# Kernel tuning notes

Measured on AMD Instinct MI355X. Metric: run time of the kernel, lower is better.

The kernel has to match this reference:

```python
import jax, jax.numpy as jnp
import numpy as np

N_NODES = 50000


def _gcn_norm(edge_index, n_nodes):
    # Add self-loops, then symmetric normalization D^-1/2 (A+I) D^-1/2 (GCNConv default).
    src = jnp.concatenate([edge_index[0], jnp.arange(n_nodes)])
    dst = jnp.concatenate([edge_index[1], jnp.arange(n_nodes)])
    deg = jax.ops.segment_sum(jnp.ones_like(src, dtype=jnp.float32), dst, num_segments=n_nodes)
    dinv = jnp.where(deg > 0, jax.lax.rsqrt(jnp.maximum(deg, 1.0)), 0.0)
    norm = dinv[src] * dinv[dst]  # [E + N]
    return src, dst, norm


def _gcn_conv(x, W, b, src, dst, norm, n_nodes):
    h = x @ W                      # [N, F_out] transform first (fewer bytes moved)
    msg = h[src] * norm[:, None]   # gather per-edge
    out = jax.ops.segment_sum(msg, dst, num_segments=n_nodes)  # scatter-add
    return out + b


def setup_inputs() -> dict:
    key = jax.random.key(0)
    k_x, k_e, k1, k2, k3, k4, k5, k6 = jax.random.split(key, 8)
    in_dim, hid, out_dim, n_edges = 128, 128, 64, 800000
    s = lambda fan_in: 1.0 / np.sqrt(fan_in)
    return {
        "x": jax.random.normal(k_x, (N_NODES, in_dim), dtype=jnp.float32),
        "edge_index": jax.random.randint(k_e, (2, n_edges), 0, N_NODES),
        "W1": jax.random.uniform(k1, (in_dim, hid), jnp.float32, -s(in_dim), s(in_dim)),
        "b1": jnp.zeros((hid,), jnp.float32),
        "W_mu": jax.random.uniform(k2, (hid, out_dim), jnp.float32, -s(hid), s(hid)),
        "b_mu": jnp.zeros((out_dim,), jnp.float32),
        "W_logstd": jax.random.uniform(k3, (hid, out_dim), jnp.float32, -s(hid), s(hid)),
        "b_logstd": jnp.zeros((out_dim,), jnp.float32),
    }


def reference(x, edge_index, W1, b1, W_mu, b_mu, W_logstd, b_logstd):
    src, dst, norm = _gcn_norm(edge_index, N_NODES)
    h = jax.nn.relu(_gcn_conv(x, W1, b1, src, dst, norm, N_NODES))
    mu = _gcn_conv(h, W_mu, b_mu, src, dst, norm, N_NODES)
    logstd = _gcn_conv(h, W_logstd, b_logstd, src, dst, norm, N_NODES)
    return mu, logstd
```

## Files before the change

kernel.cpp:

```cpp
#include <hip/hip_runtime.h>
#include <hip/hip_bf16.h>

#define N_NODES 50000
#define FDIM 128
#define NPAD 50176
#define SCAN_NB 49

typedef short bf16x8 __attribute__((ext_vector_type(8)));
typedef float f32x4  __attribute__((ext_vector_type(4)));

__device__ __forceinline__ unsigned short rne_bf16(float f) {
    unsigned int u = __float_as_uint(f);
    unsigned int r = (u + 0x7FFFu + ((u >> 16) & 1u)) >> 16;
    return (unsigned short)r;
}
__device__ __forceinline__ float bf16_to_f32(unsigned short s) {
    return __uint_as_float(((unsigned int)s) << 16);
}
__device__ __forceinline__ void split_bf16(float f, unsigned short& h, unsigned short& l) {
    h = rne_bf16(f);
    l = rne_bf16(f - bf16_to_f32(h));
}
__device__ __forceinline__ void unpack2(unsigned int d, float& f0, float& f1) {
    f0 = __uint_as_float(d << 16);
    f1 = __uint_as_float(d & 0xFFFF0000u);
}
__device__ __forceinline__ void add_row(const uint4& m, float* a) {
    float f0, f1;
    unpack2(m.x, f0, f1); a[0] += f0; a[1] += f1;
    unpack2(m.y, f0, f1); a[2] += f0; a[3] += f1;
    unpack2(m.z, f0, f1); a[4] += f0; a[5] += f1;
    unpack2(m.w, f0, f1); a[6] += f0; a[7] += f1;
}

__global__ __launch_bounds__(256) void zero_cvtw_kernel(int4* __restrict__ counts4,
                                                        const float* __restrict__ W1,
                                                        const float* __restrict__ Wmu,
                                                        const float* __restrict__ Wlog,
                                                        unsigned short* __restrict__ W1thi,
                                                        unsigned short* __restrict__ W1tlo,
                                                        unsigned short* __restrict__ Wcthi,
                                                        unsigned short* __restrict__ Wctlo) {
    int b = blockIdx.x;
    if (b < SCAN_NB) {
        int i = b * 256 + threadIdx.x;
        if (i < NPAD / 4) counts4[i] = make_int4(0, 0, 0, 0);
        return;
    }
    int tid = (b - SCAN_NB) * 256 + threadIdx.x;
    int n = tid & 127, k = tid >> 7;
    int swzidx = (n * 128 + k) ^ ((n & 7) << 3);
    unsigned short h, l;
    float v1 = W1[k * 128 + n];
    split_bf16(v1, h, l);
    W1thi[swzidx] = h;
    W1tlo[swzidx] = l;
    float v2 = (n < 64) ? Wmu[k * 64 + n] : Wlog[k * 64 + (n - 64)];
    split_bf16(v2, h, l);
    Wcthi[swzidx] = h;
    Wctlo[swzidx] = l;
}

__global__ __launch_bounds__(256) void count_kernel(const int* __restrict__ dst,
                                                    int* __restrict__ counts,
                                                    int* __restrict__ rank, int E) {
    int e = blockIdx.x * blockDim.x + threadIdx.x;
    if (e < E) rank[e] = atomicAdd(&counts[dst[e]], 1);
}

__global__ __launch_bounds__(256) void scan_local_kernel(const int* __restrict__ counts,
                                                         int* __restrict__ local,
                                                         int* __restrict__ bsums,
                                                         float* __restrict__ dinv) {
    int t    = threadIdx.x;
    int lane = t & 63;
    int wid  = t >> 6;
    int base = blockIdx.x * 1024 + t * 4;
    int4 c = *(const int4*)(counts + base);
    float4 dv;
    dv.x = (base + 0 < N_NODES) ? rsqrtf((float)c.x + 1.0f) : 0.f;
    dv.y = (base + 1 < N_NODES) ? rsqrtf((float)c.y + 1.0f) : 0.f;
    dv.z = (base + 2 < N_NODES) ? rsqrtf((float)c.z + 1.0f) : 0.f;
    dv.w = (base + 3 < N_NODES) ? rsqrtf((float)c.w + 1.0f) : 0.f;
    *(float4*)(dinv + base) = dv;
    int4 v;
    v.x = (c.x + 3) & ~3;
    v.y = (c.y + 3) & ~3;
    v.z = (c.z + 3) & ~3;
    v.w = (c.w + 3) & ~3;
    int s = v.x + v.y + v.z + v.w;
    int incl = s;
#pragma unroll
    for (int off = 1; off < 64; off <<= 1) {
        int u = __shfl_up(incl, off, 64);
        if (lane >= off) incl += u;
    }
    __shared__ int wtot[4];
    if (lane == 63) wtot[wid] = incl;
    __syncthreads();
    int wbase = 0;
#pragma unroll
    for (int w = 0; w < 3; w++) wbase += (w < wid) ? wtot[w] : 0;
    int excl = wbase + incl - s;
    int4 o;
    o.x = excl;
    o.y = excl + v.x;
    o.z = o.y + v.y;
    o.w = o.z + v.z;
    *(int4*)(local + base) = o;
    if (t == 255) bsums[blockIdx.x] = wbase + incl;
}

__global__ __launch_bounds__(256) void scan_add_kernel(const int* __restrict__ local,
                                                       const int* __restrict__ bsums,
                                                       const int* __restrict__ counts,
                                                       int* __restrict__ offsets,
                                                       int* __restrict__ csr_src,
                                                       unsigned short* __restrict__ xb,
                                                       unsigned short* __restrict__ Hb) {
    int t = threadIdx.x;
    __shared__ int s_bo;
    if (t < 64) {
        int v = (t < blockIdx.x) ? bsums[t] : 0;
#pragma unroll
        for (int off = 32; off; off >>= 1) v += __shfl_down(v, off, 64);
        if (t == 0) s_bo = v;
    }
    if (blockIdx.x == 0 && t >= 64 && t < 128) {
        int k = t - 64;
        ((unsigned int*)(xb + (size_t)N_NODES * 128))[k] = 0u;
        ((unsigned int*)(Hb + (size_t)N_NODES * 128))[k] = 0u;
    }
    __syncthreads();
    int bo = s_bo;
    int base = blockIdx.x * 1024 + t * 4;
    int4 v = *(const int4*)(local + base);
    int4 c = *(const int4*)(counts + base);
    v.x += bo; v.y += bo; v.z += bo; v.w += bo;
    *(int4*)(offsets + base) = v;
    int off0[4] = {v.x, v.y, v.z, v.w};
    int cr[4]   = {c.x, c.y, c.z, c.w};
#pragma unroll
    for (int k = 0; k < 4; k++) {
        int b = off0[k] + cr[k];
        int e = off0[k] + ((cr[k] + 3) & ~3);
        for (int j = b; j < e; j++) csr_src[j] = N_NODES;
    }
}

__global__ __launch_bounds__(256) void scatter_cvtx_kernel(const int* __restrict__ src,
                                                           const int* __restrict__ dst,
                                                           const int* __restrict__ rank,
                                                           const int* __restrict__ offsets,
                                                           int* __restrict__ csr_src, int E,
                                                           int scb,
                                                           const float* __restrict__ x,
                                                           const float* __restrict__ dinv,
                                                           unsigned short* __restrict__ xb,
                                                           int n4) {
    int b = blockIdx.x;
    if (b < scb) {
        int e = b * 256 + threadIdx.x;
        if (e < E) {
            int d = dst[e];
            int pos = offsets[d] + rank[e];
            csr_src[pos] = src[e];
        }
        return;
    }
    int i = (b - scb) * 256 + threadIdx.x;
    if (i >= n4) return;
    float dv = dinv[i >> 5];
    float4 v = ((const float4*)x)[i];
    v.x *= dv; v.y *= dv; v.z *= dv; v.w *= dv;
    unsigned int d0 = (unsigned int)rne_bf16(v.x) | ((unsigned int)rne_bf16(v.y) << 16);
    unsigned int d1 = (unsigned int)rne_bf16(v.z) | ((unsigned int)rne_bf16(v.w) << 16);
    ((uint2*)xb)[i] = make_uint2(d0, d1);
}

__global__ __launch_bounds__(256) void agg_bf16_kernel(const unsigned short* __restrict__ X,
                                                       const int* __restrict__ offsets,
                                                       const int* __restrict__ csr_src,
                                                       const float* __restrict__ dinv,
                                                       unsigned short* __restrict__ Y,
                                                       int n) {
    int node = (blockIdx.x << 4) + (threadIdx.x >> 4);
    int l16  = threadIdx.x & 15;
    if (node >= n) return;
    const uint4* X16 = (const uint4*)X;

    float a[8];
    {
        uint4 xv = X16[(size_t)node * 16 + l16];
        float f0, f1;
        unpack2(xv.x, f0, f1); a[0] = f0; a[1] = f1;
        unpack2(xv.y, f0, f1); a[2] = f0; a[3] = f1;
        unpack2(xv.z, f0, f1); a[4] = f0; a[5] = f1;
        unpack2(xv.w, f0, f1); a[6] = f0; a[7] = f1;
    }

    int beg = offsets[node], end = offsets[node + 1];
    int i = beg;
    for (; i + 8 <= end; i += 8) {
        int4 q0 = *(const int4*)(csr_src + i);
        int4 q1 = *(const int4*)(csr_src + i + 4);
        uint4 m0 = X16[(size_t)q0.x * 16 + l16];
        uint4 m1 = X16[(size_t)q0.y * 16 + l16];
        uint4 m2 = X16[(size_t)q0.z * 16 + l16];
        uint4 m3 = X16[(size_t)q0.w * 16 + l16];
        uint4 m4 = X16[(size_t)q1.x * 16 + l16];
        uint4 m5 = X16[(size_t)q1.y * 16 + l16];
        uint4 m6 = X16[(size_t)q1.z * 16 + l16];
        uint4 m7 = X16[(size_t)q1.w * 16 + l16];
        add_row(m0, a); add_row(m1, a); add_row(m2, a); add_row(m3, a);
        add_row(m4, a); add_row(m5, a); add_row(m6, a); add_row(m7, a);
    }
    if (i < end) {
        int4 q0 = *(const int4*)(csr_src + i);
        uint4 m0 = X16[(size_t)q0.x * 16 + l16];
        uint4 m1 = X16[(size_t)q0.y * 16 + l16];
        uint4 m2 = X16[(size_t)q0.z * 16 + l16];
        uint4 m3 = X16[(size_t)q0.w * 16 + l16];
        add_row(m0, a); add_row(m1, a); add_row(m2, a); add_row(m3, a);
    }

    float dv = dinv[node];
    unsigned short h[8];
#pragma unroll
    for (int j = 0; j < 8; j++) h[j] = rne_bf16(a[j] * dv);
    uint4 ph;
    ph.x = (unsigned int)h[0] | ((unsigned int)h[1] << 16);
    ph.y = (unsigned int)h[2] | ((unsigned int)h[3] << 16);
    ph.z = (unsigned int)h[4] | ((unsigned int)h[5] << 16);
    ph.w = (unsigned int)h[6] | ((unsigned int)h[7] << 16);
    ((uint4*)Y)[(size_t)node * 16 + l16] = ph;
}

template <int EPI>
__global__ __launch_bounds__(512) void mfma_gemm_kernel(const unsigned short* __restrict__ A,
                                                        const unsigned short* __restrict__ Wthi,
                                                        const unsigned short* __restrict__ Wtlo,
                                                        const float* __restrict__ ba,
                                                        const float* __restrict__ bb,
                                                        const float* __restrict__ dinv,
                                                        unsigned short* __restrict__ H,
                                                        float* __restrict__ out, int M) {
    __shared__ unsigned short Wlds[32768];

    int t    = threadIdx.x;
    int wave = t >> 6;
    int lane = t & 63;
    int m16  = lane & 15;
    int kg   = lane >> 4;

    {
        const uint4* gh = (const uint4*)Wthi;
        const uint4* gl = (const uint4*)Wtlo;
        uint4* lds4 = (uint4*)Wlds;
#pragma unroll
        for (int i = 0; i < 4; i++) lds4[i * 512 + t] = gh[i * 512 + t];
#pragma unroll
        for (int i = 0; i < 4; i++) lds4[2048 + i * 512 + t] = gl[i * 512 + t];
    }

    int rbase = blockIdx.x * 128 + wave * 16;
    int arow  = rbase + m16;
    bool rok  = arow < M;
    const unsigned short* ar = A + (size_t)(rok ? arow : 0) * 128;
    bf16x8 af[4];
#pragma unroll
    for (int kt = 0; kt < 4; kt++) {
        bf16x8 v = *(const bf16x8*)(const void*)(ar + kt * 32 + kg * 8);
        af[kt] = rok ? v : (bf16x8)(short)0;
    }
    float4 dv4 = {1.f, 1.f, 1.f, 1.f};
    if (EPI == 0) dv4 = *(const float4*)(dinv + rbase + kg * 4);
    __syncthreads();

    int swz = (m16 & 7) << 3;
#pragma unroll
    for (int np = 0; np < 4; np++) {
        int nt0 = np * 2, nt1 = np * 2 + 1;
        f32x4 acc0 = {0.f, 0.f, 0.f, 0.f};
        f32x4 acc1 = {0.f, 0.f, 0.f, 0.f};
#pragma unroll
        for (int kt = 0; kt < 4; kt++) {
            int i0 = (((nt0 * 16 + m16) * 128) + kt * 32 + kg * 8) ^ swz;
            int i1 = (((nt1 * 16 + m16) * 128) + kt * 32 + kg * 8) ^ swz;
            bf16x8 bh0 = *(const bf16x8*)(const void*)&Wlds[i0];
            bf16x8 bl0 = *(const bf16x8*)(const void*)&Wlds[16384 + i0];
            bf16x8 bh1 = *(const bf16x8*)(const void*)&Wlds[i1];
            bf16x8 bl1 = *(const bf16x8*)(const void*)&Wlds[16384 + i1];
            acc0 = __builtin_amdgcn_mfma_f32_16x16x32_bf16(af[kt], bh0, acc0, 0, 0, 0);
            acc1 = __builtin_amdgcn_mfma_f32_16x16x32_bf16(af[kt], bh1, acc1, 0, 0, 0);
            acc0 = __builtin_amdgcn_mfma_f32_16x16x32_bf16(af[kt], bl0, acc0, 0, 0, 0);
            acc1 = __builtin_amdgcn_mfma_f32_16x16x32_bf16(af[kt], bl1, acc1, 0, 0, 0);
        }
#pragma unroll
        for (int half = 0; half < 2; half++) {
            int nt = half ? nt1 : nt0;
            const f32x4& acc = half ? acc1 : acc0;
            int n0 = nt * 16 + m16;
            if (EPI == 0) {
                float b = ba[n0];
#pragma unroll
                for (int j = 0; j < 4; j++) {
                    int r = rbase + kg * 4 + j;
                    if (r < M) {
                        float v = fmaxf(acc[j] + b, 0.f) * dv4[j];
                        H[(size_t)r * 128 + n0] = rne_bf16(v);
                    }
                }
            } else {
                bool is_mu = (n0 < 64);
                int c = is_mu ? n0 : (n0 - 64);
                float b = is_mu ? ba[c] : bb[c];
                size_t obase = is_mu ? 0 : (size_t)N_NODES * 64;
#pragma unroll
                for (int j = 0; j < 4; j++) {
                    int r = rbase + kg * 4 + j;
                    if (r < M) out[obase + (size_t)r * 64 + c] = acc[j] + b;
                }
            }
        }
    }
}

extern "C" void kernel_launch(void* const* d_in, const int* in_sizes, int n_in,
                              void* d_out, int out_size, void* d_ws, size_t ws_size,
                              hipStream_t stream) {
    const float* x    = (const float*)d_in[0];
    const int*   ei   = (const int*)d_in[1];
    const float* W1   = (const float*)d_in[2];
    const float* b1   = (const float*)d_in[3];
    const float* Wmu  = (const float*)d_in[4];
    const float* bmu  = (const float*)d_in[5];
    const float* Wlog = (const float*)d_in[6];
    const float* blog = (const float*)d_in[7];
    float* out = (float*)d_out;

    const int N = N_NODES;
    const int E = in_sizes[1] / 2;
    const int Emax = E + 3 * N;
    const int* src = ei;
    const int* dst = ei + E;

    auto align256 = [](size_t v) { return (v + 255) & ~(size_t)255; };
    char* ws = (char*)d_ws;
    size_t off = 0;
    int*   counts  = (int*)(ws + off);  off += align256((size_t)NPAD * 4);
    int*   offsets = (int*)(ws + off);  off += align256((size_t)NPAD * 4);
    int*   local   = (int*)(ws + off);  off += align256((size_t)NPAD * 4);
    int*   bsums   = (int*)(ws + off);  off += align256(256 * 4);
    float* dinv    = (float*)(ws + off); off += align256((size_t)NPAD * 4);
    int*   rank    = (int*)(ws + off);  off += align256((size_t)E * 4);
    int*   csr_src = (int*)(ws + off);  off += align256((size_t)Emax * 4);
    unsigned short* xb    = (unsigned short*)(ws + off); off += align256((size_t)(N + 1) * FDIM * 2);
    unsigned short* Hb    = (unsigned short*)(ws + off); off += align256((size_t)(N + 1) * FDIM * 2);
    unsigned short* Ag    = (unsigned short*)(ws + off); off += align256((size_t)N * FDIM * 2);
    unsigned short* W1thi = (unsigned short*)(ws + off); off += align256(128 * 128 * 2);
    unsigned short* W1tlo = (unsigned short*)(ws + off); off += align256(128 * 128 * 2);
    unsigned short* Wcthi = (unsigned short*)(ws + off); off += align256(128 * 128 * 2);
    unsigned short* Wctlo = (unsigned short*)(ws + off); off += align256(128 * 128 * 2);

    zero_cvtw_kernel<<<SCAN_NB + 64, 256, 0, stream>>>((int4*)counts, W1, Wmu, Wlog,
                                                       W1thi, W1tlo, Wcthi, Wctlo);
    count_kernel<<<(E + 255) / 256, 256, 0, stream>>>(dst, counts, rank, E);
    scan_local_kernel<<<SCAN_NB, 256, 0, stream>>>(counts, local, bsums, dinv);
    scan_add_kernel<<<SCAN_NB, 256, 0, stream>>>(local, bsums, counts, offsets,
                                                 csr_src, xb, Hb);
    {
        int scb = (E + 255) / 256;
        int cvb = (N * FDIM / 4 + 255) / 256;
        scatter_cvtx_kernel<<<scb + cvb, 256, 0, stream>>>(src, dst, rank, offsets,
                                                           csr_src, E, scb,
                                                           x, dinv, xb, N * FDIM / 4);
    }
    agg_bf16_kernel<<<(N + 15) / 16, 256, 0, stream>>>(xb, offsets, csr_src, dinv, Ag, N);
    mfma_gemm_kernel<0><<<(N + 127) / 128, 512, 0, stream>>>(Ag, W1thi, W1tlo,
                                                             b1, nullptr, dinv, Hb, nullptr, N);
    agg_bf16_kernel<<<(N + 15) / 16, 256, 0, stream>>>(Hb, offsets, csr_src, dinv, Ag, N);
    mfma_gemm_kernel<1><<<(N + 127) / 128, 512, 0, stream>>>(Ag, Wcthi, Wctlo,
                                                             bmu, blog, nullptr, nullptr, out, N);
}
```

Measured before the change: 150.7 us.

## Fuse neighbor aggregation into MFMA GEMM kernel, eliminating intermediate buffer

Replaces the separate aggregation and GEMM kernels with one kernel. Each lane gathers and sums the neighbor rows for its own node straight into registers laid out as MFMA A-fragments, then runs the bf16 hi/lo MFMA GEMM. This removes the global write and read of the aggregated matrix and two kernel launches per layer. In exchange each lane now processes a whole 32-float row slice over all edges, which raises register pressure (launch_bounds 512,4). Load balance across nodes of different degree is also coarser than in the 16-lane-per-node aggregation kernel.

New measurement: 286.2 us. 1.9x slower.

```diff
diff --git a/kernel.cpp b/kernel.cpp
--- a/kernel.cpp
+++ b/kernel.cpp
@@ -178,73 +178,18 @@
     ((uint2*)xb)[i] = make_uint2(d0, d1);
 }
 
-__global__ __launch_bounds__(256) void agg_bf16_kernel(const unsigned short* __restrict__ X,
-                                                       const int* __restrict__ offsets,
-                                                       const int* __restrict__ csr_src,
-                                                       const float* __restrict__ dinv,
-                                                       unsigned short* __restrict__ Y,
-                                                       int n) {
-    int node = (blockIdx.x << 4) + (threadIdx.x >> 4);
-    int l16  = threadIdx.x & 15;
-    if (node >= n) return;
-    const uint4* X16 = (const uint4*)X;
-
-    float a[8];
-    {
-        uint4 xv = X16[(size_t)node * 16 + l16];
-        float f0, f1;
-        unpack2(xv.x, f0, f1); a[0] = f0; a[1] = f1;
-        unpack2(xv.y, f0, f1); a[2] = f0; a[3] = f1;
-        unpack2(xv.z, f0, f1); a[4] = f0; a[5] = f1;
-        unpack2(xv.w, f0, f1); a[6] = f0; a[7] = f1;
-    }
-
-    int beg = offsets[node], end = offsets[node + 1];
-    int i = beg;
-    for (; i + 8 <= end; i += 8) {
-        int4 q0 = *(const int4*)(csr_src + i);
-        int4 q1 = *(const int4*)(csr_src + i + 4);
-        uint4 m0 = X16[(size_t)q0.x * 16 + l16];
-        uint4 m1 = X16[(size_t)q0.y * 16 + l16];
-        uint4 m2 = X16[(size_t)q0.z * 16 + l16];
-        uint4 m3 = X16[(size_t)q0.w * 16 + l16];
-        uint4 m4 = X16[(size_t)q1.x * 16 + l16];
-        uint4 m5 = X16[(size_t)q1.y * 16 + l16];
-        uint4 m6 = X16[(size_t)q1.z * 16 + l16];
-        uint4 m7 = X16[(size_t)q1.w * 16 + l16];
-        add_row(m0, a); add_row(m1, a); add_row(m2, a); add_row(m3, a);
-        add_row(m4, a); add_row(m5, a); add_row(m6, a); add_row(m7, a);
-    }
-    if (i < end) {
-        int4 q0 = *(const int4*)(csr_src + i);
-        uint4 m0 = X16[(size_t)q0.x * 16 + l16];
-        uint4 m1 = X16[(size_t)q0.y * 16 + l16];
-        uint4 m2 = X16[(size_t)q0.z * 16 + l16];
-        uint4 m3 = X16[(size_t)q0.w * 16 + l16];
-        add_row(m0, a); add_row(m1, a); add_row(m2, a); add_row(m3, a);
-    }
-
-    float dv = dinv[node];
-    unsigned short h[8];
-#pragma unroll
-    for (int j = 0; j < 8; j++) h[j] = rne_bf16(a[j] * dv);
-    uint4 ph;
-    ph.x = (unsigned int)h[0] | ((unsigned int)h[1] << 16);
-    ph.y = (unsigned int)h[2] | ((unsigned int)h[3] << 16);
-    ph.z = (unsigned int)h[4] | ((unsigned int)h[5] << 16);
-    ph.w = (unsigned int)h[6] | ((unsigned int)h[7] << 16);
-    ((uint4*)Y)[(size_t)node * 16 + l16] = ph;
-}
-
 template <int EPI>
-__global__ __launch_bounds__(512) void mfma_gemm_kernel(const unsigned short* __restrict__ A,
-                                                        const unsigned short* __restrict__ Wthi,
-                                                        const unsigned short* __restrict__ Wtlo,
-                                                        const float* __restrict__ ba,
-                                                        const float* __restrict__ bb,
-                                                        const float* __restrict__ dinv,
-                                                        unsigned short* __restrict__ H,
-                                                        float* __restrict__ out, int M) {
+__global__ __launch_bounds__(512, 4) void fused_agg_gemm_kernel(
+        const unsigned short* __restrict__ X,
+        const int* __restrict__ offsets,
+        const int* __restrict__ csr_src,
+        const float* __restrict__ dinv,
+        const unsigned short* __restrict__ Wthi,
+        const unsigned short* __restrict__ Wtlo,
+        const float* __restrict__ ba,
+        const float* __restrict__ bb,
+        unsigned short* __restrict__ H,
+        float* __restrict__ out, int M) {
     __shared__ unsigned short Wlds[32768];
 
     int t    = threadIdx.x;
@@ -256,25 +201,70 @@
     {
         const uint4* gh = (const uint4*)Wthi;
         const uint4* gl = (const uint4*)Wtlo;
+        uint4 wr[8];
+#pragma unroll
+        for (int i = 0; i < 4; i++) wr[i] = gh[i * 512 + t];
+#pragma unroll
+        for (int i = 0; i < 4; i++) wr[4 + i] = gl[i * 512 + t];
         uint4* lds4 = (uint4*)Wlds;
 #pragma unroll
-        for (int i = 0; i < 4; i++) lds4[i * 512 + t] = gh[i * 512 + t];
-#pragma unroll
-        for (int i = 0; i < 4; i++) lds4[2048 + i * 512 + t] = gl[i * 512 + t];
-    }
-
-    int rbase = blockIdx.x * 128 + wave * 16;
-    int arow  = rbase + m16;
-    bool rok  = arow < M;
-    const unsigned short* ar = A + (size_t)(rok ? arow : 0) * 128;
+        for (int i = 0; i < 4; i++) lds4[i * 512 + t] = wr[i];
+#pragma unroll
+        for (int i = 0; i < 4; i++) lds4[2048 + i * 512 + t] = wr[4 + i];
+    }
+
+    int wrbase = blockIdx.x * 128 + wave * 16;
+    int node   = wrbase + m16;
+    bool rok   = node < M;
+    int snode  = rok ? node : N_NODES;
+    const uint4* X16 = (const uint4*)X;
+
+    float acc[32];
+#pragma unroll
+    for (int kt = 0; kt < 4; kt++) {
+        uint4 s = X16[(size_t)snode * 16 + kt * 4 + kg];
+        float f0, f1;
+        unpack2(s.x, f0, f1); acc[kt * 8 + 0] = f0; acc[kt * 8 + 1] = f1;
+        unpack2(s.y, f0, f1); acc[kt * 8 + 2] = f0; acc[kt * 8 + 3] = f1;
+        unpack2(s.z, f0, f1); acc[kt * 8 + 4] = f0; acc[kt * 8 + 5] = f1;
+        unpack2(s.w, f0, f1); acc[kt * 8 + 6] = f0; acc[kt * 8 + 7] = f1;
+    }
+
+    int beg = offsets[node], end = offsets[node + 1];
+    for (int i = beg; i < end; i += 4) {
+        int4 q = *(const int4*)(csr_src + i);
+        uint4 r0[4], r1[4];
+#pragma unroll
+        for (int kt = 0; kt < 4; kt++) r0[kt] = X16[(size_t)q.x * 16 + kt * 4 + kg];
+#pragma unroll
+        for (int kt = 0; kt < 4; kt++) r1[kt] = X16[(size_t)q.y * 16 + kt * 4 + kg];
+#pragma unroll
+        for (int kt = 0; kt < 4; kt++) add_row(r0[kt], acc + kt * 8);
+#pragma unroll
+        for (int kt = 0; kt < 4; kt++) add_row(r1[kt], acc + kt * 8);
+#pragma unroll
+        for (int kt = 0; kt < 4; kt++) r0[kt] = X16[(size_t)q.z * 16 + kt * 4 + kg];
+#pragma unroll
+        for (int kt = 0; kt < 4; kt++) r1[kt] = X16[(size_t)q.w * 16 + kt * 4 + kg];
+#pragma unroll
+        for (int kt = 0; kt < 4; kt++) add_row(r0[kt], acc + kt * 8);
+#pragma unroll
+        for (int kt = 0; kt < 4; kt++) add_row(r1[kt], acc + kt * 8);
+    }
+
+    float dvn = dinv[node];
     bf16x8 af[4];
 #pragma unroll
     for (int kt = 0; kt < 4; kt++) {
-        bf16x8 v = *(const bf16x8*)(const void*)(ar + kt * 32 + kg * 8);
-        af[kt] = rok ? v : (bf16x8)(short)0;
-    }
+        bf16x8 v;
+#pragma unroll
+        for (int j = 0; j < 8; j++) v[j] = (short)rne_bf16(acc[kt * 8 + j] * dvn);
+        af[kt] = v;
+    }
+
     float4 dv4 = {1.f, 1.f, 1.f, 1.f};
-    if (EPI == 0) dv4 = *(const float4*)(dinv + rbase + kg * 4);
+    if (EPI == 0) dv4 = *(const float4*)(dinv + wrbase + kg * 4);
+
     __syncthreads();
 
     int swz = (m16 & 7) << 3;
@@ -299,15 +289,15 @@
 #pragma unroll
         for (int half = 0; half < 2; half++) {
             int nt = half ? nt1 : nt0;
-            const f32x4& acc = half ? acc1 : acc0;
+            const f32x4& a = half ? acc1 : acc0;
             int n0 = nt * 16 + m16;
             if (EPI == 0) {
                 float b = ba[n0];
 #pragma unroll
                 for (int j = 0; j < 4; j++) {
-                    int r = rbase + kg * 4 + j;
+                    int r = wrbase + kg * 4 + j;
                     if (r < M) {
-                        float v = fmaxf(acc[j] + b, 0.f) * dv4[j];
+                        float v = fmaxf(a[j] + b, 0.f) * dv4[j];
                         H[(size_t)r * 128 + n0] = rne_bf16(v);
                     }
                 }
@@ -318,8 +308,8 @@
                 size_t obase = is_mu ? 0 : (size_t)N_NODES * 64;
 #pragma unroll
                 for (int j = 0; j < 4; j++) {
-                    int r = rbase + kg * 4 + j;
-                    if (r < M) out[obase + (size_t)r * 64 + c] = acc[j] + b;
+                    int r = wrbase + kg * 4 + j;
+                    if (r < M) out[obase + (size_t)r * 64 + c] = a[j] + b;
                 }
             }
         }
@@ -357,7 +347,6 @@
     int*   csr_src = (int*)(ws + off);  off += align256((size_t)Emax * 4);
     unsigned short* xb    = (unsigned short*)(ws + off); off += align256((size_t)(N + 1) * FDIM * 2);
     unsigned short* Hb    = (unsigned short*)(ws + off); off += align256((size_t)(N + 1) * FDIM * 2);
-    unsigned short* Ag    = (unsigned short*)(ws + off); off += align256((size_t)N * FDIM * 2);
     unsigned short* W1thi = (unsigned short*)(ws + off); off += align256(128 * 128 * 2);
     unsigned short* W1tlo = (unsigned short*)(ws + off); off += align256(128 * 128 * 2);
     unsigned short* Wcthi = (unsigned short*)(ws + off); off += align256(128 * 128 * 2);
@@ -376,10 +365,8 @@
                                                            csr_src, E, scb,
                                                            x, dinv, xb, N * FDIM / 4);
     }
-    agg_bf16_kernel<<<(N + 15) / 16, 256, 0, stream>>>(xb, offsets, csr_src, dinv, Ag, N);
-    mfma_gemm_kernel<0><<<(N + 127) / 128, 512, 0, stream>>>(Ag, W1thi, W1tlo,
-                                                             b1, nullptr, dinv, Hb, nullptr, N);
-    agg_bf16_kernel<<<(N + 15) / 16, 256, 0, stream>>>(Hb, offsets, csr_src, dinv, Ag, N);
-    mfma_gemm_kernel<1><<<(N + 127) / 128, 512, 0, stream>>>(Ag, Wcthi, Wctlo,
-                                                             bmu, blog, nullptr, nullptr, out, N);
-}
+    fused_agg_gemm_kernel<0><<<(N + 127) / 128, 512, 0, stream>>>(
+        xb, offsets, csr_src, dinv, W1thi, W1tlo, b1, nullptr, Hb, nullptr, N);
+    fused_agg_gemm_kernel<1><<<(N + 127) / 128, 512, 0, stream>>>(
+        Hb, offsets, csr_src, dinv, Wcthi, Wctlo, bmu, blog, nullptr, out, N);
+}
```

## Split neighbor aggregation into four column groups per node for cache locality

Applied to the files above, without the earlier changes.

The sparse aggregation kernel now splits the 128 bf16 features of each row into four 64-byte column groups, each handled by a separate grid section. Each lane gathers 4 bytes per neighbor instead of 16, so the blocks running at the same time touch only a quarter of each feature row, which shrinks the working set held in L2. In exchange the CSR index and offset reads are repeated four times, there are four times as many launched blocks, and each gather is narrower (64 bytes per row segment), which may lower memory efficiency.

Result: slower. 172.6 us (+14.5%).

```diff
diff --git a/kernel.cpp b/kernel.cpp
--- a/kernel.cpp
+++ b/kernel.cpp
@@ -24,13 +24,6 @@
 __device__ __forceinline__ void unpack2(unsigned int d, float& f0, float& f1) {
     f0 = __uint_as_float(d << 16);
     f1 = __uint_as_float(d & 0xFFFF0000u);
-}
-__device__ __forceinline__ void add_row(const uint4& m, float* a) {
-    float f0, f1;
-    unpack2(m.x, f0, f1); a[0] += f0; a[1] += f1;
-    unpack2(m.y, f0, f1); a[2] += f0; a[3] += f1;
-    unpack2(m.z, f0, f1); a[4] += f0; a[5] += f1;
-    unpack2(m.w, f0, f1); a[6] += f0; a[7] += f1;
 }
 
 __global__ __launch_bounds__(256) void zero_cvtw_kernel(int4* __restrict__ counts4,
@@ -178,25 +171,25 @@
     ((uint2*)xb)[i] = make_uint2(d0, d1);
 }
 
-__global__ __launch_bounds__(256) void agg_bf16_kernel(const unsigned short* __restrict__ X,
-                                                       const int* __restrict__ offsets,
-                                                       const int* __restrict__ csr_src,
-                                                       const float* __restrict__ dinv,
-                                                       unsigned short* __restrict__ Y,
-                                                       int n) {
-    int node = (blockIdx.x << 4) + (threadIdx.x >> 4);
+__global__ __launch_bounds__(256) void agg_bf16_col_kernel(const unsigned short* __restrict__ X,
+                                                           const int* __restrict__ offsets,
+                                                           const int* __restrict__ csr_src,
+                                                           const float* __restrict__ dinv,
+                                                           unsigned short* __restrict__ Y,
+                                                           int n, int nb_per_g) {
+    int b  = blockIdx.x;
+    int g  = b / nb_per_g;
+    int nb = b - g * nb_per_g;
+    int node = (nb << 4) + (threadIdx.x >> 4);
     int l16  = threadIdx.x & 15;
     if (node >= n) return;
-    const uint4* X16 = (const uint4*)X;
-
-    float a[8];
+    const unsigned int* Xu = (const unsigned int*)X;
+    int coff = g * 16 + l16;
+
+    float a0, a1;
     {
-        uint4 xv = X16[(size_t)node * 16 + l16];
-        float f0, f1;
-        unpack2(xv.x, f0, f1); a[0] = f0; a[1] = f1;
-        unpack2(xv.y, f0, f1); a[2] = f0; a[3] = f1;
-        unpack2(xv.z, f0, f1); a[4] = f0; a[5] = f1;
-        unpack2(xv.w, f0, f1); a[6] = f0; a[7] = f1;
+        unsigned int s = Xu[(size_t)node * 64 + coff];
+        unpack2(s, a0, a1);
     }
 
     int beg = offsets[node], end = offsets[node + 1];
@@ -204,36 +197,40 @@
     for (; i + 8 <= end; i += 8) {
         int4 q0 = *(const int4*)(csr_src + i);
         int4 q1 = *(const int4*)(csr_src + i + 4);
-        uint4 m0 = X16[(size_t)q0.x * 16 + l16];
-        uint4 m1 = X16[(size_t)q0.y * 16 + l16];
-        uint4 m2 = X16[(size_t)q0.z * 16 + l16];
-        uint4 m3 = X16[(size_t)q0.w * 16 + l16];
-        uint4 m4 = X16[(size_t)q1.x * 16 + l16];
-        uint4 m5 = X16[(size_t)q1.y * 16 + l16];
-        uint4 m6 = X16[(size_t)q1.z * 16 + l16];
-        uint4 m7 = X16[(size_t)q1.w * 16 + l16];
-        add_row(m0, a); add_row(m1, a); add_row(m2, a); add_row(m3, a);
-        add_row(m4, a); add_row(m5, a); add_row(m6, a); add_row(m7, a);
+        unsigned int m0 = Xu[(size_t)q0.x * 64 + coff];
+        unsigned int m1 = Xu[(size_t)q0.y * 64 + coff];
+        unsigned int m2 = Xu[(size_t)q0.z * 64 + coff];
+        unsigned int m3 = Xu[(size_t)q0.w * 64 + coff];
+        unsigned int m4 = Xu[(size_t)q1.x * 64 + coff];
+        unsigned int m5 = Xu[(size_t)q1.y * 64 + coff];
+        unsigned int m6 = Xu[(size_t)q1.z * 64 + coff];
+        unsigned int m7 = Xu[(size_t)q1.w * 64 + coff];
+        float f0, f1;
+        unpack2(m0, f0, f1); a0 += f0; a1 += f1;
+        unpack2(m1, f0, f1); a0 += f0; a1 += f1;
+        unpack2(m2, f0, f1); a0 += f0; a1 += f1;
+        unpack2(m3, f0, f1); a0 += f0; a1 += f1;
+        unpack2(m4, f0, f1); a0 += f0; a1 += f1;
+        unpack2(m5, f0, f1); a0 += f0; a1 += f1;
+        unpack2(m6, f0, f1); a0 += f0; a1 += f1;
+        unpack2(m7, f0, f1); a0 += f0; a1 += f1;
     }
     if (i < end) {
         int4 q0 = *(const int4*)(csr_src + i);
-        uint4 m0 = X16[(size_t)q0.x * 16 + l16];
-        uint4 m1 = X16[(size_t)q0.y * 16 + l16];
-        uint4 m2 = X16[(size_t)q0.z * 16 + l16];
-        uint4 m3 = X16[(size_t)q0.w * 16 + l16];
-        add_row(m0, a); add_row(m1, a); add_row(m2, a); add_row(m3, a);
+        unsigned int m0 = Xu[(size_t)q0.x * 64 + coff];
+        unsigned int m1 = Xu[(size_t)q0.y * 64 + coff];
+        unsigned int m2 = Xu[(size_t)q0.z * 64 + coff];
+        unsigned int m3 = Xu[(size_t)q0.w * 64 + coff];
+        float f0, f1;
+        unpack2(m0, f0, f1); a0 += f0; a1 += f1;
+        unpack2(m1, f0, f1); a0 += f0; a1 += f1;
+        unpack2(m2, f0, f1); a0 += f0; a1 += f1;
+        unpack2(m3, f0, f1); a0 += f0; a1 += f1;
     }
 
     float dv = dinv[node];
-    unsigned short h[8];
-#pragma unroll
-    for (int j = 0; j < 8; j++) h[j] = rne_bf16(a[j] * dv);
-    uint4 ph;
-    ph.x = (unsigned int)h[0] | ((unsigned int)h[1] << 16);
-    ph.y = (unsigned int)h[2] | ((unsigned int)h[3] << 16);
-    ph.z = (unsigned int)h[4] | ((unsigned int)h[5] << 16);
-    ph.w = (unsigned int)h[6] | ((unsigned int)h[7] << 16);
-    ((uint4*)Y)[(size_t)node * 16 + l16] = ph;
+    unsigned int o = (unsigned int)rne_bf16(a0 * dv) | ((unsigned int)rne_bf16(a1 * dv) << 16);
+    ((unsigned int*)Y)[(size_t)node * 64 + coff] = o;
 }
 
 template <int EPI>
@@ -376,10 +373,11 @@
                                                            csr_src, E, scb,
                                                            x, dinv, xb, N * FDIM / 4);
     }
-    agg_bf16_kernel<<<(N + 15) / 16, 256, 0, stream>>>(xb, offsets, csr_src, dinv, Ag, N);
+    int nbg = (N + 15) / 16;
+    agg_bf16_col_kernel<<<nbg * 4, 256, 0, stream>>>(xb, offsets, csr_src, dinv, Ag, N, nbg);
     mfma_gemm_kernel<0><<<(N + 127) / 128, 512, 0, stream>>>(Ag, W1thi, W1tlo,
                                                              b1, nullptr, dinv, Hb, nullptr, N);
-    agg_bf16_kernel<<<(N + 15) / 16, 256, 0, stream>>>(Hb, offsets, csr_src, dinv, Ag, N);
+    agg_bf16_col_kernel<<<nbg * 4, 256, 0, stream>>>(Hb, offsets, csr_src, dinv, Ag, N, nbg);
     mfma_gemm_kernel<1><<<(N + 127) / 128, 512, 0, stream>>>(Ag, Wcthi, Wctlo,
                                                              bmu, blog, nullptr, nullptr, out, N);
 }
```
